# Performance work log

Hardware: AMD Instinct MI355X
Metric: run time of the kernel (lower is better)

## Reference

```python
import jax, jax.numpy as jnp
import numpy as np
from jax import lax

N, D, H = 8192, 256, 128
EPS = 1e-5


def _layernorm(x, g, b):
    m = jnp.mean(x, axis=-1, keepdims=True)
    v = jnp.mean((x - m) ** 2, axis=-1, keepdims=True)
    return (x - m) * jax.lax.rsqrt(v + EPS) * g + b


def setup_inputs() -> dict:
    key = jax.random.key(0)
    ks = jax.random.split(key, 8)
    s = 1.0 / np.sqrt(D)
    return {
        "x": jax.random.normal(ks[0], (N, D), jnp.float32),
        "wq": jax.random.normal(ks[1], (D, D), jnp.float32) * s,
        "bq": jnp.zeros((D,), jnp.float32),
        "wk": jax.random.normal(ks[2], (D, D), jnp.float32) * s,
        "bk": jnp.zeros((D,), jnp.float32),
        "wv": jax.random.normal(ks[3], (D, D), jnp.float32) * s,
        "bv": jnp.zeros((D,), jnp.float32),
        "cw": jax.random.normal(ks[4], (1, 1, 3, 3), jnp.float32) / 3.0,
        "cb": jnp.zeros((1,), jnp.float32),
        "m1w": jax.random.normal(ks[5], (H, D), jnp.float32) * s,
        "m2w": jax.random.normal(ks[6], (D, H), jnp.float32) / np.sqrt(H),
        "bng": jnp.ones((H,), jnp.float32),
        "bnb": jnp.zeros((H,), jnp.float32),
        "ln1g": jnp.ones((D,), jnp.float32),
        "ln1b": jnp.zeros((D,), jnp.float32),
        "ln2g": jnp.ones((D,), jnp.float32),
        "ln2b": jnp.zeros((D,), jnp.float32),
    }


def reference(x, wq, bq, wk, bk, wv, bv, cw, cb, m1w, m2w, bng, bnb, ln1g, ln1b, ln2g, ln2b):
    q = x @ wq.T + bq            # [N, D]
    k = x @ wk.T + bk
    v = x @ wv.T + bv
    # global Frobenius-norm normalization (torch.norm(q, p=2) over whole tensor)
    q = q / jnp.linalg.norm(q)
    k = k / jnp.linalg.norm(k)
    A = q @ k.T                  # [N, N]
    # 3x3 conv2d, 1->1 channel, padding SAME
    A4 = A[None, None, :, :]
    A4 = lax.conv_general_dilated(A4, cw, window_strides=(1, 1), padding="SAME")
    A4 = A4 + cb[None, :, None, None]
    agg_A = A4[0, 0]             # [N, N]
    attn = agg_A @ v             # [N, D]
    h = x + _layernorm(attn, ln1g, ln1b)
    # MLP with BatchNorm1d (training-mode batch stats, biased var)
    z = _layernorm(h, ln2g, ln2b) @ m1w.T          # [N, H]
    mu = jnp.mean(z, axis=0)
    var = jnp.mean((z - mu) ** 2, axis=0)
    z = (z - mu) * jax.lax.rsqrt(var + EPS) * bng + bnb
    z = jax.nn.relu(z)
    out = h + z @ m2w.T
    return out
```

## Files before the change

kernel.cpp:

```cpp
#include <hip/hip_runtime.h>
#include <hip/hip_bf16.h>
#include <math.h>


#define N_ 8192
#define D_ 256
#define H_ 128
#define EPSF 1e-5f

typedef unsigned short ushort_t;
typedef unsigned int uint_t;
typedef __attribute__((ext_vector_type(8))) short bf16x8;
typedef __attribute__((ext_vector_type(4))) short bf16x4;
typedef __attribute__((ext_vector_type(4))) float f32x4;

static const size_t OFF_QB  = 0;
static const size_t OFF_KT  = 4195328;
static const size_t OFF_VT  = 8389632;
static const size_t OFF_GP  = 12588032;
static const size_t OFF_MT  = 25170944;
static const size_t OFF_SVP = 25564160;
static const size_t OFF_SVC = 25826304;
static const size_t OFF_RED = 25827328;
static const size_t OFF_ZSP = 25829376;
static const size_t OFF_BNS = 26353664;
static const size_t OFF_WC  = 26354688;
static const size_t OFF_M1C = 26747904;
static const size_t OFF_M2C = 26813440;
static const size_t WS_NEED = 26878976;

#define VT_S 8200

__device__ __forceinline__ ushort_t f2bf(float f) {
    __hip_bfloat16 h = __float2bfloat16(f);
    return reinterpret_cast<ushort_t&>(h);
}

__device__ __forceinline__ bf16x8 cvt8(float4 f0, float4 f1) {
    bf16x8 o;
    o[0] = (short)f2bf(f0.x); o[1] = (short)f2bf(f0.y);
    o[2] = (short)f2bf(f0.z); o[3] = (short)f2bf(f0.w);
    o[4] = (short)f2bf(f1.x); o[5] = (short)f2bf(f1.y);
    o[6] = (short)f2bf(f1.z); o[7] = (short)f2bf(f1.w);
    return o;
}

__device__ __forceinline__ float waveSum(float v)
{
#pragma unroll
    for (int o = 32; o > 0; o >>= 1) v += __shfl_xor(v, o);
    return v;
}

__global__ void prep_w(const float* __restrict__ wq, const float* __restrict__ wk,
                       const float* __restrict__ wv, const float* __restrict__ m1w,
                       const float* __restrict__ m2w,
                       ushort_t* __restrict__ WC, ushort_t* __restrict__ M1C,
                       ushort_t* __restrict__ M2C,
                       ushort_t* __restrict__ QbG, ushort_t* __restrict__ VT)
{
    const int bid = blockIdx.x, tid = threadIdx.x;
    if (bid < 96) {
        const int sel = bid >> 5, kb = bid & 31;
        const float* W = (sel == 0) ? wq : ((sel == 1) ? wk : wv);
        const float* p = W + (size_t)tid * 256 + kb * 8;
        *(bf16x8*)(WC + (size_t)sel * 65536 + (size_t)kb * 2048 + (size_t)tid * 8)
            = cvt8(*(const float4*)p, *(const float4*)(p + 4));
    } else if (bid < 128) {
        const int kb = bid - 96;
        if (tid < 128) {
            const float* p = m1w + (size_t)tid * 256 + kb * 8;
            *(bf16x8*)(M1C + (size_t)kb * 1024 + (size_t)tid * 8)
                = cvt8(*(const float4*)p, *(const float4*)(p + 4));
        }
    } else if (bid < 144) {
        const int kb = bid - 128;
        const float* p = m2w + (size_t)tid * 128 + kb * 8;
        *(bf16x8*)(M2C + (size_t)kb * 2048 + (size_t)tid * 8)
            = cvt8(*(const float4*)p, *(const float4*)(p + 4));
    } else {
        QbG[tid] = 0; QbG[(size_t)8193 * 256 + tid] = 0;
        VT[(size_t)tid * VT_S] = 0; VT[(size_t)tid * VT_S + 8193] = 0;
    }
}

__global__ void __launch_bounds__(256)
qkv_mfma(const float* __restrict__ x, const ushort_t* __restrict__ WC,
         const float* __restrict__ bq, const float* __restrict__ bk,
         const float* __restrict__ bv,
         ushort_t* __restrict__ QbG, ushort_t* __restrict__ KT,
         ushort_t* __restrict__ VT,
         float* __restrict__ RED, float* __restrict__ SVP)
{
    __shared__ ushort_t XS[32][264];
    __shared__ float lds4[4];
    const int tid = threadIdx.x, lane = tid & 63, wid = tid >> 6;
    const int sel = blockIdx.y;
    const int i0 = blockIdx.x * 32;
    const int jw = wid * 64;
    const int l15 = lane & 15, kg = lane >> 4;
    const ushort_t* Wc = WC + (size_t)sel * 65536;
    const float* B = (sel == 0) ? bq : ((sel == 1) ? bk : bv);

#pragma unroll
    for (int p = 0; p < 4; ++p) {
        int lin = p * 256 + tid;
        int row = lin >> 5;
        int c8  = (lin & 31) * 8;
        const float* xp = x + (size_t)(i0 + row) * 256 + c8;
        *(bf16x8*)(&XS[row][c8]) = cvt8(*(const float4*)xp, *(const float4*)(xp + 4));
    }
    __syncthreads();

    f32x4 acc[2][4];
#pragma unroll
    for (int mi = 0; mi < 2; ++mi)
#pragma unroll
        for (int ni = 0; ni < 4; ++ni) acc[mi][ni] = 0.0f;

    for (int k0 = 0; k0 < 256; k0 += 32) {
        bf16x8 a[2], b[4];
#pragma unroll
        for (int mi = 0; mi < 2; ++mi)
            a[mi] = *(const bf16x8*)(&XS[16 * mi + l15][k0 + 8 * kg]);
#pragma unroll
        for (int ni = 0; ni < 4; ++ni)
            b[ni] = *(const bf16x8*)(Wc + (size_t)((k0 >> 3) + kg) * 2048
                                        + (size_t)(jw + 16 * ni + l15) * 8);
#pragma unroll
        for (int mi = 0; mi < 2; ++mi)
#pragma unroll
            for (int ni = 0; ni < 4; ++ni)
                acc[mi][ni] = __builtin_amdgcn_mfma_f32_16x16x32_bf16(a[mi], b[ni], acc[mi][ni], 0, 0, 0);
    }

    float ssq = 0.0f;
    float colp[4] = {0.0f, 0.0f, 0.0f, 0.0f};

    if (sel == 0) {
#pragma unroll
        for (int mi = 0; mi < 2; ++mi)
#pragma unroll
            for (int ni = 0; ni < 4; ++ni) {
                const int col = jw + 16 * ni + l15;
                const float bias = B[col];
#pragma unroll
                for (int r = 0; r < 4; ++r) {
                    const int row = i0 + 16 * mi + 4 * kg + r;
                    float val = acc[mi][ni][r] + bias;
                    QbG[(size_t)(row + 1) * 256 + col] = f2bf(val);
                    ssq = fmaf(val, val, ssq);
                }
            }
    } else if (sel == 1) {
#pragma unroll
        for (int mi = 0; mi < 2; ++mi)
#pragma unroll
            for (int ni = 0; ni < 4; ++ni) {
                const int col = jw + 16 * ni + l15;
                const float bias = B[col];
                const int tb = i0 + 16 * mi + 4 * kg;
                bf16x4 pk;
#pragma unroll
                for (int r = 0; r < 4; ++r) {
                    float val = acc[mi][ni][r] + bias;
                    ssq = fmaf(val, val, ssq);
                    pk[r] = (short)f2bf(val);
                }
                *(bf16x4*)(KT + (size_t)col * 8192 + tb) = pk;
            }
    } else {
#pragma unroll
        for (int mi = 0; mi < 2; ++mi)
#pragma unroll
            for (int ni = 0; ni < 4; ++ni) {
                const int col = jw + 16 * ni + l15;
                const float bias = B[col];
                const int tb = i0 + 16 * mi + 4 * kg;
                float v0 = acc[mi][ni][0] + bias, v1 = acc[mi][ni][1] + bias;
                float v2 = acc[mi][ni][2] + bias, v3 = acc[mi][ni][3] + bias;
                colp[ni] += v0 + v1 + v2 + v3;
                ushort_t* p = VT + (size_t)col * VT_S + tb + 1;
                p[0] = f2bf(v0);
                *(uint_t*)(p + 1) = (uint_t)f2bf(v1) | ((uint_t)f2bf(v2) << 16);
                p[3] = f2bf(v3);
            }
    }

    if (sel < 2) {
        float s = ssq;
#pragma unroll
        for (int o = 32; o > 0; o >>= 1) s += __shfl_down(s, o);
        if (lane == 0) lds4[wid] = s;
        __syncthreads();
        if (tid == 0)
            RED[sel * 256 + blockIdx.x] = lds4[0] + lds4[1] + lds4[2] + lds4[3];
    } else {
#pragma unroll
        for (int ni = 0; ni < 4; ++ni) {
            float v = colp[ni];
            v += __shfl_xor(v, 16);
            v += __shfl_xor(v, 32);
            if (kg == 0)
                SVP[(size_t)blockIdx.x * 256 + jw + 16 * ni + l15] = v;
        }
    }
}

__global__ void __launch_bounds__(256)
g_mfma(const ushort_t* __restrict__ KT, const ushort_t* __restrict__ VT,
       float* __restrict__ GP)
{
    const int tid = threadIdx.x, lane = tid & 63, wid = tid >> 6;
    const int d0 = blockIdx.x * 64 + (wid >> 1) * 32;
    const int jw = blockIdx.y * 32 + (wid & 1) * 16;
    const int ks = blockIdx.z;
    const int l15 = lane & 15, kg = lane >> 4;

    f32x4 acc[3][2];
#pragma unroll
    for (int v = 0; v < 3; ++v) { acc[v][0] = 0.0f; acc[v][1] = 0.0f; }

    for (int tt = 0; tt < 512; tt += 32) {
        const int t0 = ks * 512 + tt;
        bf16x8 a[2];
#pragma unroll
        for (int mi = 0; mi < 2; ++mi)
            a[mi] = *(const bf16x8*)(KT + (size_t)(d0 + 16 * mi + l15) * 8192 + t0 + 8 * kg);

        const ushort_t* vp = VT + (size_t)(jw + l15) * VT_S + t0 + 8 * kg;
        uint4 r0 = *(const uint4*)vp;
        uint4 r2 = *(const uint4*)(vp + 2);
        uint4 m1;
        m1.x = (r0.x >> 16) | (r2.x << 16);
        m1.y = (r0.y >> 16) | (r2.y << 16);
        m1.z = (r0.z >> 16) | (r2.z << 16);
        m1.w = (r0.w >> 16) | (r2.w << 16);
        bf16x8 b2 = __builtin_bit_cast(bf16x8, r0);
        bf16x8 b0 = __builtin_bit_cast(bf16x8, r2);
        bf16x8 b1 = __builtin_bit_cast(bf16x8, m1);
#pragma unroll
        for (int mi = 0; mi < 2; ++mi) {
            acc[0][mi] = __builtin_amdgcn_mfma_f32_16x16x32_bf16(a[mi], b0, acc[0][mi], 0, 0, 0);
            acc[1][mi] = __builtin_amdgcn_mfma_f32_16x16x32_bf16(a[mi], b1, acc[1][mi], 0, 0, 0);
            acc[2][mi] = __builtin_amdgcn_mfma_f32_16x16x32_bf16(a[mi], b2, acc[2][mi], 0, 0, 0);
        }
    }

#pragma unroll
    for (int v = 0; v < 3; ++v) {
        float* gp = GP + (size_t)(ks * 3 + v) * 65536;
#pragma unroll
        for (int mi = 0; mi < 2; ++mi)
#pragma unroll
            for (int r = 0; r < 4; ++r)
                gp[(size_t)(d0 + 16 * mi + 4 * kg + r) * 256 + (jw + l15)]
                    = acc[v][mi][r];
    }
}

__global__ void combine_m(const float* __restrict__ GP, const float* __restrict__ cw,
                          const float* __restrict__ RED, const float* __restrict__ SVP,
                          const float* __restrict__ cb,
                          ushort_t* __restrict__ MTc, float* __restrict__ SVC)
{
    __shared__ float lds8[8];
    __shared__ float scsh;
    const int d = blockIdx.x, j = threadIdx.x;

    float sq = RED[j], sk = RED[256 + j];
#pragma unroll
    for (int o = 32; o > 0; o >>= 1) { sq += __shfl_down(sq, o); sk += __shfl_down(sk, o); }
    if ((j & 63) == 0) { lds8[j >> 6] = sq; lds8[4 + (j >> 6)] = sk; }

    float g[3] = {0.0f, 0.0f, 0.0f};
    for (int ks = 0; ks < 16; ++ks)
#pragma unroll
        for (int v = 0; v < 3; ++v)
            g[v] += GP[(size_t)(ks * 3 + v) * 65536 + (size_t)d * 256 + j];

    __syncthreads();
    if (j == 0) {
        float SQ = lds8[0] + lds8[1] + lds8[2] + lds8[3];
        float SK = lds8[4] + lds8[5] + lds8[6] + lds8[7];
        scsh = rsqrtf(SQ) * rsqrtf(SK);
    }
    __syncthreads();
    const float sc = scsh;

#pragma unroll
    for (int u = 0; u < 3; ++u) {
        float m = sc * (cw[u * 3 + 0] * g[0] + cw[u * 3 + 1] * g[1] + cw[u * 3 + 2] * g[2]);
        MTc[(size_t)u * 65536 + (size_t)(d >> 3) * 2048 + (size_t)j * 8 + (d & 7)]
            = f2bf(m);
    }
    if (d == 0) {
        float s = 0.0f;
        for (int b = 0; b < 256; ++b) s += SVP[(size_t)b * 256 + j];
        SVC[j] = cb[0] * s;
    }
}

__global__ void __launch_bounds__(512)
attn_ln_z_mfma(const ushort_t* __restrict__ QbG, const ushort_t* __restrict__ MTc,
               const float* __restrict__ SVC, const float* __restrict__ x,
               const float* __restrict__ ln1g, const float* __restrict__ ln1b,
               const float* __restrict__ ln2g, const float* __restrict__ ln2b,
               const ushort_t* __restrict__ M1C,
               float* __restrict__ h, float* __restrict__ Z,
               float* __restrict__ ZSP)
{
    __shared__ ushort_t QS[18][264];
    __shared__ float OUT[16][260];
    const int tid = threadIdx.x, lane = tid & 63, wid = tid >> 6;
    const int i0 = blockIdx.x * 16;
    const int jw = wid * 32;
    const int l15 = lane & 15, kg = lane >> 4;

    float4 xpre0 = *(const float4*)(x + (size_t)(i0 + wid * 2 + 0) * 256 + lane * 4);
    float4 xpre1 = *(const float4*)(x + (size_t)(i0 + wid * 2 + 1) * 256 + lane * 4);

    {
        int row = tid >> 5, c8 = (tid & 31) * 8;
        *(bf16x8*)(&QS[row][c8]) = *(const bf16x8*)(QbG + (size_t)(i0 + row) * 256 + c8);
        int idx = tid + 512;
        if (idx < 576) {
            row = idx >> 5; c8 = (idx & 31) * 8;
            *(bf16x8*)(&QS[row][c8]) = *(const bf16x8*)(QbG + (size_t)(i0 + row) * 256 + c8);
        }
    }
    __syncthreads();

    f32x4 acc[2];
    acc[0] = 0.0f; acc[1] = 0.0f;

    for (int k0 = 0; k0 < 256; k0 += 32) {
        bf16x8 a[3], b[3][2];
#pragma unroll
        for (int u = 0; u < 3; ++u)
            a[u] = *(const bf16x8*)(&QS[l15 + u][k0 + 8 * kg]);
#pragma unroll
        for (int u = 0; u < 3; ++u)
#pragma unroll
            for (int ni = 0; ni < 2; ++ni)
                b[u][ni] = *(const bf16x8*)(MTc + (size_t)u * 65536
                    + (size_t)((k0 >> 3) + kg) * 2048
                    + (size_t)(jw + 16 * ni + l15) * 8);
#pragma unroll
        for (int ni = 0; ni < 2; ++ni)
#pragma unroll
            for (int u = 0; u < 3; ++u)
                acc[ni] = __builtin_amdgcn_mfma_f32_16x16x32_bf16(
                    a[u], b[u][ni], acc[ni], 0, 0, 0);
    }

#pragma unroll
    for (int ni = 0; ni < 2; ++ni) {
        const int col = jw + 16 * ni + l15;
        const float sv = SVC[col];
#pragma unroll
        for (int r = 0; r < 4; ++r)
            OUT[4 * kg + r][col] = acc[ni][r] + sv;
    }
    __syncthreads();

    const float4 g14 = *(const float4*)(ln1g + lane * 4);
    const float4 b14 = *(const float4*)(ln1b + lane * 4);
    const float4 g24 = *(const float4*)(ln2g + lane * 4);
    const float4 b24 = *(const float4*)(ln2b + lane * 4);
#pragma unroll
    for (int rr = 0; rr < 2; ++rr) {
        const int row_l = wid * 2 + rr;
        const size_t off = (size_t)(i0 + row_l) * 256 + lane * 4;

        float4 a4 = *(const float4*)&OUT[row_l][lane * 4];
        float m = waveSum(a4.x + a4.y + a4.z + a4.w) * (1.0f / D_);
        float4 d4 = make_float4(a4.x - m, a4.y - m, a4.z - m, a4.w - m);
        float var = waveSum(d4.x * d4.x + d4.y * d4.y + d4.z * d4.z + d4.w * d4.w) * (1.0f / D_);
        float rs = rsqrtf(var + EPSF);

        float4 x4 = (rr == 0) ? xpre0 : xpre1;
        float4 h4;
        h4.x = x4.x + d4.x * rs * g14.x + b14.x;
        h4.y = x4.y + d4.y * rs * g14.y + b14.y;
        h4.z = x4.z + d4.z * rs * g14.z + b14.z;
        h4.w = x4.w + d4.w * rs * g14.w + b14.w;
        *(float4*)(h + off) = h4;

        float m2 = waveSum(h4.x + h4.y + h4.z + h4.w) * (1.0f / D_);
        float4 e4 = make_float4(h4.x - m2, h4.y - m2, h4.z - m2, h4.w - m2);
        float v2 = waveSum(e4.x * e4.x + e4.y * e4.y + e4.z * e4.z + e4.w * e4.w) * (1.0f / D_);
        float rs2 = rsqrtf(v2 + EPSF);

        float4 o4;
        o4.x = e4.x * rs2 * g24.x + b24.x;
        o4.y = e4.y * rs2 * g24.y + b24.y;
        o4.z = e4.z * rs2 * g24.z + b24.z;
        o4.w = e4.w * rs2 * g24.w + b24.w;
        *(float4*)&OUT[row_l][lane * 4] = o4;
    }
    __syncthreads();

    const int jz = wid * 16;
    f32x4 zacc;
    zacc = 0.0f;

    for (int k0 = 0; k0 < 256; k0 += 32) {
        bf16x8 a, b;
        {
            const float* lp = &OUT[l15][k0 + 8 * kg];
            a = cvt8(*(const float4*)lp, *(const float4*)(lp + 4));
        }
        b = *(const bf16x8*)(M1C + (size_t)((k0 >> 3) + kg) * 1024
                                  + (size_t)(jz + l15) * 8);
        zacc = __builtin_amdgcn_mfma_f32_16x16x32_bf16(a, b, zacc, 0, 0, 0);
    }

    float s = 0.0f, q = 0.0f;
    const int col = jz + l15;
#pragma unroll
    for (int r = 0; r < 4; ++r) {
        float zv = zacc[r];
        Z[(size_t)(i0 + 4 * kg + r) * 128 + col] = zv;
        s += zv;
        q = fmaf(zv, zv, q);
    }
    s += __shfl_xor(s, 16); s += __shfl_xor(s, 32);
    q += __shfl_xor(q, 16); q += __shfl_xor(q, 32);
    if (kg == 0) {
        ZSP[(size_t)blockIdx.x * 256 + col] = s;
        ZSP[(size_t)blockIdx.x * 256 + 128 + col] = q;
    }
}

__global__ void bn_reduce(const float* __restrict__ ZSP, float* __restrict__ BNS)
{
    __shared__ float red[8][32];
    const int tid = threadIdx.x;
    const int c0 = blockIdx.x * 32;
    const int cl = tid & 31, g = tid >> 5;
    float s = 0.0f;
    for (int b = g; b < 512; b += 8)
        s += ZSP[(size_t)b * 256 + c0 + cl];
    red[g][cl] = s;
    __syncthreads();
    if (tid < 32) {
        float t = 0.0f;
#pragma unroll
        for (int g2 = 0; g2 < 8; ++g2) t += red[g2][tid];
        BNS[c0 + tid] = t;
    }
}

__global__ void __launch_bounds__(512)
gemm_out_mfma(const float* __restrict__ Z, const ushort_t* __restrict__ M2C,
              const float* __restrict__ BNS,
              const float* __restrict__ bng, const float* __restrict__ bnb,
              float* __restrict__ out)
{
    __shared__ float bnA[128], bnB[128];
    __shared__ ushort_t XS[16][136];
    const int tid = threadIdx.x, lane = tid & 63, wid = tid >> 6;
    const int i0 = blockIdx.x * 16;
    const int jw = wid * 32;
    const int l15 = lane & 15, kg = lane >> 4;

    float oprev[2][4];
#pragma unroll
    for (int ni = 0; ni < 2; ++ni)
#pragma unroll
        for (int r = 0; r < 4; ++r)
            oprev[ni][r] = out[(size_t)(i0 + 4 * kg + r) * 256 + jw + 16 * ni + l15];

    if (tid < 128) {
        float s = BNS[tid], q = BNS[128 + tid];
        float mu = s * (1.0f / N_);
        float var = q * (1.0f / N_) - mu * mu;
        float aa = rsqrtf(var + EPSF) * bng[tid];
        bnA[tid] = aa;
        bnB[tid] = bnb[tid] - mu * aa;
    }
    __syncthreads();

    if (tid < 256) {
        int row = tid >> 4, c8 = (tid & 15) * 8;
        const float* zp = Z + (size_t)(i0 + row) * 128 + c8;
        float4 f0 = *(const float4*)zp;
        float4 f1 = *(const float4*)(zp + 4);
        float4 g0, g1;
        g0.x = fmaxf(fmaf(f0.x, bnA[c8 + 0], bnB[c8 + 0]), 0.0f);
        g0.y = fmaxf(fmaf(f0.y, bnA[c8 + 1], bnB[c8 + 1]), 0.0f);
        g0.z = fmaxf(fmaf(f0.z, bnA[c8 + 2], bnB[c8 + 2]), 0.0f);
        g0.w = fmaxf(fmaf(f0.w, bnA[c8 + 3], bnB[c8 + 3]), 0.0f);
        g1.x = fmaxf(fmaf(f1.x, bnA[c8 + 4], bnB[c8 + 4]), 0.0f);
        g1.y = fmaxf(fmaf(f1.y, bnA[c8 + 5], bnB[c8 + 5]), 0.0f);
        g1.z = fmaxf(fmaf(f1.z, bnA[c8 + 6], bnB[c8 + 6]), 0.0f);
        g1.w = fmaxf(fmaf(f1.w, bnA[c8 + 7], bnB[c8 + 7]), 0.0f);
        *(bf16x8*)(&XS[row][c8]) = cvt8(g0, g1);
    }
    __syncthreads();

    f32x4 acc[2];
    acc[0] = 0.0f; acc[1] = 0.0f;

    for (int k0 = 0; k0 < 128; k0 += 32) {
        bf16x8 a = *(const bf16x8*)(&XS[l15][k0 + 8 * kg]);
        bf16x8 b[2];
#pragma unroll
        for (int ni = 0; ni < 2; ++ni)
            b[ni] = *(const bf16x8*)(M2C + (size_t)((k0 >> 3) + kg) * 2048
                                          + (size_t)(jw + 16 * ni + l15) * 8);
#pragma unroll
        for (int ni = 0; ni < 2; ++ni)
            acc[ni] = __builtin_amdgcn_mfma_f32_16x16x32_bf16(a, b[ni], acc[ni], 0, 0, 0);
    }

#pragma unroll
    for (int ni = 0; ni < 2; ++ni)
#pragma unroll
        for (int r = 0; r < 4; ++r) {
            const size_t idx = (size_t)(i0 + 4 * kg + r) * 256
                             + (jw + 16 * ni + l15);
            out[idx] = oprev[ni][r] + acc[ni][r];
        }
}

extern "C" void kernel_launch(void* const* d_in, const int* in_sizes, int n_in,
                              void* d_out, int out_size, void* d_ws, size_t ws_size,
                              hipStream_t stream)
{
    const float* x    = (const float*)d_in[0];
    const float* wq   = (const float*)d_in[1];
    const float* bq   = (const float*)d_in[2];
    const float* wk   = (const float*)d_in[3];
    const float* bk   = (const float*)d_in[4];
    const float* wv   = (const float*)d_in[5];
    const float* bv   = (const float*)d_in[6];
    const float* cw   = (const float*)d_in[7];
    const float* cb   = (const float*)d_in[8];
    const float* m1w  = (const float*)d_in[9];
    const float* m2w  = (const float*)d_in[10];
    const float* bng  = (const float*)d_in[11];
    const float* bnb  = (const float*)d_in[12];
    const float* ln1g = (const float*)d_in[13];
    const float* ln1b = (const float*)d_in[14];
    const float* ln2g = (const float*)d_in[15];
    const float* ln2b = (const float*)d_in[16];

    float* outF = (float*)d_out;
    char*  wsb  = (char*)d_ws;
    if (ws_size < WS_NEED) return;

    ushort_t* QbG = (ushort_t*)(wsb + OFF_QB);
    ushort_t* KT  = (ushort_t*)(wsb + OFF_KT);
    ushort_t* VT  = (ushort_t*)(wsb + OFF_VT);
    float*    GP  = (float*)(wsb + OFF_GP);
    ushort_t* MTc = (ushort_t*)(wsb + OFF_MT);
    float*    SVP = (float*)(wsb + OFF_SVP);
    float*    SVC = (float*)(wsb + OFF_SVC);
    float*    RED = (float*)(wsb + OFF_RED);
    float*    ZSP = (float*)(wsb + OFF_ZSP);
    float*    BNS = (float*)(wsb + OFF_BNS);
    ushort_t* WC  = (ushort_t*)(wsb + OFF_WC);
    ushort_t* M1C = (ushort_t*)(wsb + OFF_M1C);
    ushort_t* M2C = (ushort_t*)(wsb + OFF_M2C);
    float*    Z   = (float*)(wsb + OFF_GP);

    const dim3 b256(256);
    const dim3 b512(512);

    prep_w<<<145, b256, 0, stream>>>(wq, wk, wv, m1w, m2w, WC, M1C, M2C, QbG, VT);
    qkv_mfma<<<dim3(256, 3), b256, 0, stream>>>(x, WC, bq, bk, bv,
                                                QbG, KT, VT, RED, SVP);
    g_mfma<<<dim3(4, 8, 16), b256, 0, stream>>>(KT, VT, GP);
    combine_m<<<256, b256, 0, stream>>>(GP, cw, RED, SVP, cb, MTc, SVC);
    attn_ln_z_mfma<<<512, b512, 0, stream>>>(QbG, MTc, SVC, x,
                                             ln1g, ln1b, ln2g, ln2b, M1C,
                                             outF, Z, ZSP);
    bn_reduce<<<8, b256, 0, stream>>>(ZSP, BNS);
    gemm_out_mfma<<<512, b512, 0, stream>>>(Z, M2C, BNS, bng, bnb, outF);
}
```

Measured before the change: 88.57 us.

## Block K and V transposes into 8-element chunks and pre-convert x to bf16

K and V are now stored chunk-blocked: for every group of 8 tokens, all 256 columns are laid out contiguously. This replaces the long row-strided KT/VT layouts, so g_mfma loads should be coalesced and V's shifted windows come from one 16-byte load plus one 4-byte load. x is converted to bf16 once in prep_w, so qkv_mfma's three sel blocks no longer each reconvert the fp32 rows. The cost is extra workspace, a larger prep launch, and boundary-special-case stores in the V writer.

After: 82.08 us. 1.08x faster.

```diff
diff --git a/kernel.cpp b/kernel.cpp
--- a/kernel.cpp
+++ b/kernel.cpp
@@ -27,9 +27,8 @@
 static const size_t OFF_WC  = 26354688;
 static const size_t OFF_M1C = 26747904;
 static const size_t OFF_M2C = 26813440;
-static const size_t WS_NEED = 26878976;
-
-#define VT_S 8200
+static const size_t OFF_XB  = 26878976;
+static const size_t WS_NEED = 31073280;
 
 __device__ __forceinline__ ushort_t f2bf(float f) {
     __hip_bfloat16 h = __float2bfloat16(f);
@@ -54,10 +53,10 @@
 
 __global__ void prep_w(const float* __restrict__ wq, const float* __restrict__ wk,
                        const float* __restrict__ wv, const float* __restrict__ m1w,
-                       const float* __restrict__ m2w,
+                       const float* __restrict__ m2w, const float* __restrict__ x,
                        ushort_t* __restrict__ WC, ushort_t* __restrict__ M1C,
-                       ushort_t* __restrict__ M2C,
-                       ushort_t* __restrict__ QbG, ushort_t* __restrict__ VT)
+                       ushort_t* __restrict__ M2C, ushort_t* __restrict__ XB,
+                       ushort_t* __restrict__ QbG, ushort_t* __restrict__ VTC)
 {
     const int bid = blockIdx.x, tid = threadIdx.x;
     if (bid < 96) {
@@ -78,18 +77,23 @@
         const float* p = m2w + (size_t)tid * 128 + kb * 8;
         *(bf16x8*)(M2C + (size_t)kb * 2048 + (size_t)tid * 8)
             = cvt8(*(const float4*)p, *(const float4*)(p + 4));
+    } else if (bid == 144) {
+        QbG[tid] = 0; QbG[(size_t)8193 * 256 + tid] = 0;
+        VTC[(size_t)tid * 8] = 0;
+        VTC[((size_t)1024 * 256 + tid) * 8 + 1] = 0;
     } else {
-        QbG[tid] = 0; QbG[(size_t)8193 * 256 + tid] = 0;
-        VT[(size_t)tid * VT_S] = 0; VT[(size_t)tid * VT_S + 8193] = 0;
+        const size_t lin = (size_t)(bid - 145) * 2048 + (size_t)tid * 8;
+        const float* p = x + lin;
+        *(bf16x8*)(XB + lin) = cvt8(*(const float4*)p, *(const float4*)(p + 4));
     }
 }
 
 __global__ void __launch_bounds__(256)
-qkv_mfma(const float* __restrict__ x, const ushort_t* __restrict__ WC,
+qkv_mfma(const ushort_t* __restrict__ XB, const ushort_t* __restrict__ WC,
          const float* __restrict__ bq, const float* __restrict__ bk,
          const float* __restrict__ bv,
-         ushort_t* __restrict__ QbG, ushort_t* __restrict__ KT,
-         ushort_t* __restrict__ VT,
+         ushort_t* __restrict__ QbG, ushort_t* __restrict__ KTC,
+         ushort_t* __restrict__ VTC,
          float* __restrict__ RED, float* __restrict__ SVP)
 {
     __shared__ ushort_t XS[32][264];
@@ -107,8 +111,7 @@
         int lin = p * 256 + tid;
         int row = lin >> 5;
         int c8  = (lin & 31) * 8;
-        const float* xp = x + (size_t)(i0 + row) * 256 + c8;
-        *(bf16x8*)(&XS[row][c8]) = cvt8(*(const float4*)xp, *(const float4*)(xp + 4));
+        *(bf16x8*)(&XS[row][c8]) = *(const bf16x8*)(XB + (size_t)(i0 + row) * 256 + c8);
     }
     __syncthreads();
 
@@ -167,7 +170,7 @@
                     ssq = fmaf(val, val, ssq);
                     pk[r] = (short)f2bf(val);
                 }
-                *(bf16x4*)(KT + (size_t)col * 8192 + tb) = pk;
+                *(bf16x4*)(KTC + ((size_t)(tb >> 3) * 256 + col) * 8 + (tb & 7)) = pk;
             }
     } else {
 #pragma unroll
@@ -177,13 +180,18 @@
                 const int col = jw + 16 * ni + l15;
                 const float bias = B[col];
                 const int tb = i0 + 16 * mi + 4 * kg;
+                const int cb = tb >> 3, e0 = (tb & 7) + 1;
                 float v0 = acc[mi][ni][0] + bias, v1 = acc[mi][ni][1] + bias;
                 float v2 = acc[mi][ni][2] + bias, v3 = acc[mi][ni][3] + bias;
                 colp[ni] += v0 + v1 + v2 + v3;
-                ushort_t* p = VT + (size_t)col * VT_S + tb + 1;
+                ushort_t* p = VTC + ((size_t)cb * 256 + col) * 8 + e0;
                 p[0] = f2bf(v0);
                 *(uint_t*)(p + 1) = (uint_t)f2bf(v1) | ((uint_t)f2bf(v2) << 16);
-                p[3] = f2bf(v3);
+                ushort_t v3b = f2bf(v3);
+                if (e0 == 5)
+                    VTC[((size_t)(cb + 1) * 256 + col) * 8] = v3b;
+                else
+                    p[3] = v3b;
             }
     }
 
@@ -208,7 +216,7 @@
 }
 
 __global__ void __launch_bounds__(256)
-g_mfma(const ushort_t* __restrict__ KT, const ushort_t* __restrict__ VT,
+g_mfma(const ushort_t* __restrict__ KTC, const ushort_t* __restrict__ VTC,
        float* __restrict__ GP)
 {
     const int tid = threadIdx.x, lane = tid & 63, wid = tid >> 6;
@@ -223,14 +231,17 @@
 
     for (int tt = 0; tt < 512; tt += 32) {
         const int t0 = ks * 512 + tt;
+        const int cb0 = (t0 >> 3) + kg;
         bf16x8 a[2];
 #pragma unroll
         for (int mi = 0; mi < 2; ++mi)
-            a[mi] = *(const bf16x8*)(KT + (size_t)(d0 + 16 * mi + l15) * 8192 + t0 + 8 * kg);
-
-        const ushort_t* vp = VT + (size_t)(jw + l15) * VT_S + t0 + 8 * kg;
-        uint4 r0 = *(const uint4*)vp;
-        uint4 r2 = *(const uint4*)(vp + 2);
+            a[mi] = *(const bf16x8*)(KTC + ((size_t)cb0 * 256 + (d0 + 16 * mi + l15)) * 8);
+
+        const int j = jw + l15;
+        uint4 r0 = *(const uint4*)(VTC + ((size_t)cb0 * 256 + j) * 8);
+        uint_t rx = *(const uint_t*)(VTC + ((size_t)(cb0 + 1) * 256 + j) * 8);
+        uint4 r2;
+        r2.x = r0.y; r2.y = r0.z; r2.z = r0.w; r2.w = rx;
         uint4 m1;
         m1.x = (r0.x >> 16) | (r2.x << 16);
         m1.y = (r0.y >> 16) | (r2.y << 16);
@@ -552,8 +563,8 @@
     if (ws_size < WS_NEED) return;
 
     ushort_t* QbG = (ushort_t*)(wsb + OFF_QB);
-    ushort_t* KT  = (ushort_t*)(wsb + OFF_KT);
-    ushort_t* VT  = (ushort_t*)(wsb + OFF_VT);
+    ushort_t* KTC = (ushort_t*)(wsb + OFF_KT);
+    ushort_t* VTC = (ushort_t*)(wsb + OFF_VT);
     float*    GP  = (float*)(wsb + OFF_GP);
     ushort_t* MTc = (ushort_t*)(wsb + OFF_MT);
     float*    SVP = (float*)(wsb + OFF_SVP);
@@ -564,15 +575,17 @@
     ushort_t* WC  = (ushort_t*)(wsb + OFF_WC);
     ushort_t* M1C = (ushort_t*)(wsb + OFF_M1C);
     ushort_t* M2C = (ushort_t*)(wsb + OFF_M2C);
+    ushort_t* XB  = (ushort_t*)(wsb + OFF_XB);
     float*    Z   = (float*)(wsb + OFF_GP);
 
     const dim3 b256(256);
     const dim3 b512(512);
 
-    prep_w<<<145, b256, 0, stream>>>(wq, wk, wv, m1w, m2w, WC, M1C, M2C, QbG, VT);
-    qkv_mfma<<<dim3(256, 3), b256, 0, stream>>>(x, WC, bq, bk, bv,
-                                                QbG, KT, VT, RED, SVP);
-    g_mfma<<<dim3(4, 8, 16), b256, 0, stream>>>(KT, VT, GP);
+    prep_w<<<1169, b256, 0, stream>>>(wq, wk, wv, m1w, m2w, x,
+                                      WC, M1C, M2C, XB, QbG, VTC);
+    qkv_mfma<<<dim3(256, 3), b256, 0, stream>>>(XB, WC, bq, bk, bv,
+                                                QbG, KTC, VTC, RED, SVP);
+    g_mfma<<<dim3(4, 8, 16), b256, 0, stream>>>(KTC, VTC, GP);
     combine_m<<<256, b256, 0, stream>>>(GP, cw, RED, SVP, cb, MTc, SVC);
     attn_ln_z_mfma<<<512, b512, 0, stream>>>(QbG, MTc, SVC, x,
                                              ln1g, ln1b, ln2g, ln2b, M1C,
```
